# Performance work log

Hardware: AMD Instinct MI355X
Metric: run time of the kernel (lower is better)

The kernel has to match this reference:

```python
import jax, jax.numpy as jnp
import numpy as np

N_EMBD = 1024
N_EXPERTS = 8
TOP_K = 2
D_FF = 4 * N_EMBD


def setup_inputs() -> dict:
    key = jax.random.key(0)
    ks = jax.random.split(key, 6)
    B, S = 4, 2048
    s = 1.0 / np.sqrt(N_EMBD)
    sf = 1.0 / np.sqrt(D_FF)
    x = jax.random.normal(ks[0], (B, S, N_EMBD), dtype=jnp.float32)
    router_w = jax.random.uniform(ks[1], (N_EMBD, N_EXPERTS), minval=-s, maxval=s, dtype=jnp.float32)
    wfc = jax.random.uniform(ks[2], (N_EXPERTS, N_EMBD, D_FF), minval=-s, maxval=s, dtype=jnp.float32)
    bfc = jax.random.uniform(ks[3], (N_EXPERTS, D_FF), minval=-s, maxval=s, dtype=jnp.float32)
    wproj = jax.random.uniform(ks[4], (N_EXPERTS, D_FF, N_EMBD), minval=-sf, maxval=sf, dtype=jnp.float32)
    bproj = jax.random.uniform(ks[5], (N_EXPERTS, N_EMBD), minval=-sf, maxval=sf, dtype=jnp.float32)
    return {"x": x, "router_w": router_w, "wfc": wfc, "bfc": bfc, "wproj": wproj, "bproj": bproj}


def reference(x, router_w, wfc, bfc, wproj, bproj):
    B, S, D = x.shape
    E = wfc.shape[0]
    xf = x.reshape(-1, D)  # [N, D] tokens
    logits = xf @ router_w  # [N, E]
    probs = jax.nn.softmax(logits.astype(jnp.float32), axis=-1)
    w, sel = jax.lax.top_k(probs, TOP_K)  # [N, K]
    w = w / jnp.sum(w, axis=-1, keepdims=True)  # norm_topk_prob
    w = w.astype(x.dtype)
    out = jnp.zeros_like(xf)
    for e in range(E):
        # per-token gate for expert e (0 if not routed here) -- same math as
        # gather -> MLP -> weighted scatter-add in the original
        gate = jnp.sum(jnp.where(sel == e, w, jnp.zeros_like(w)), axis=-1)  # [N]
        h = jax.nn.gelu(xf @ wfc[e] + bfc[e], approximate=False)  # [N, 4D]
        y = h @ wproj[e] + bproj[e]  # [N, D]
        out = out + gate[:, None] * y
    return out.reshape(B, S, D)
```

## Files before the change

### kernel.cpp

```cpp
#include <hip/hip_runtime.h>
#include <hip/hip_bf16.h>


#define N_TOK 8192
#define DMODEL 1024
#define NEXP 8
#define DFF 4096
#define CAP 8192
#define MAXW 136

typedef __attribute__((ext_vector_type(8))) short short8;
typedef __attribute__((ext_vector_type(4))) float f32x4;

#define GLOAD_LDS16(g, l)                                              \
  __builtin_amdgcn_global_load_lds(                                    \
      (const __attribute__((address_space(1))) unsigned int*)(g),      \
      (__attribute__((address_space(3))) unsigned int*)(l), 16, 0, 0)

__device__ __forceinline__ unsigned short f2bf(float f) {
  unsigned u = __float_as_uint(f);
  return (unsigned short)((u + 0x7FFFu + ((u >> 16) & 1u)) >> 16);
}

__device__ __forceinline__ float gelu_f(float v) {
  return 0.5f * v * (1.0f + erff(v * 0.70710678118654752f));
}

__global__ void router_k(const float* __restrict__ x, const float* __restrict__ rw,
                         int* __restrict__ cnt, int* __restrict__ tok,
                         float* __restrict__ gate, unsigned short* __restrict__ xb) {
  int lane = threadIdx.x & 63;
  int t = blockIdx.x * 4 + (threadIdx.x >> 6);
  const float* xr = x + (size_t)t * DMODEL;
  unsigned short* xbr = xb + (size_t)t * DMODEL;
  float p[8];
#pragma unroll
  for (int e = 0; e < 8; ++e) p[e] = 0.0f;
#pragma unroll
  for (int j = 0; j < DMODEL / 64; ++j) {
    int i = lane + j * 64;
    float xv = xr[i];
    xbr[i] = f2bf(xv);
    const float4* r = (const float4*)(rw + (size_t)i * 8);
    float4 a = r[0], b = r[1];
    p[0] += xv * a.x; p[1] += xv * a.y; p[2] += xv * a.z; p[3] += xv * a.w;
    p[4] += xv * b.x; p[5] += xv * b.y; p[6] += xv * b.z; p[7] += xv * b.w;
  }
#pragma unroll
  for (int e = 0; e < 8; ++e) {
#pragma unroll
    for (int off = 32; off; off >>= 1) p[e] += __shfl_xor(p[e], off, 64);
  }
  if (lane == 0) {
    int e1 = 0;
#pragma unroll
    for (int e = 1; e < 8; ++e) if (p[e] > p[e1]) e1 = e;
    int e2 = (e1 == 0) ? 1 : 0;
#pragma unroll
    for (int e = 0; e < 8; ++e) if (e != e1 && p[e] > p[e2]) e2 = e;
    float w1 = 1.0f / (1.0f + expf(p[e2] - p[e1]));
    float w2 = 1.0f - w1;
    int s1 = atomicAdd(&cnt[e1], 1);
    tok[e1 * CAP + s1] = t; gate[e1 * CAP + s1] = w1;
    int s2 = atomicAdd(&cnt[e2], 1);
    tok[e2 * CAP + s2] = t; gate[e2 * CAP + s2] = w2;
  }
}

__global__ void prefix_k(const int* __restrict__ cnt, int* __restrict__ off,
                         int* __restrict__ nwork, int* __restrict__ wl) {
  if (threadIdx.x == 0 && blockIdx.x == 0) {
    int s = 0, n = 0;
    for (int e = 0; e < NEXP; ++e) {
      off[e] = s;
      int ntile = (cnt[e] + 127) >> 7;
      for (int mt = 0; mt < ntile; ++mt) wl[n++] = (e << 16) | mt;
      s += cnt[e];
    }
    nwork[0] = n;
  }
}

__global__ __launch_bounds__(256) void cvt_wt_k(const float* __restrict__ W,
                                                unsigned short* __restrict__ WT,
                                                int K, int N) {
  __shared__ float ls[64][68];
  int b = blockIdx.x;
  int nkt = K >> 6, nnt = N >> 6;
  int kt = b % nkt;
  int nt = (b / nkt) % nnt;
  int e = b / (nkt * nnt);
  const float* Wb = W + (size_t)e * K * N + (size_t)(kt * 64) * N + nt * 64;
  int t = threadIdx.x;
  int nn = (t & 15) * 4, kr = t >> 4;
#pragma unroll
  for (int i = 0; i < 4; ++i) {
    float4 v = *(const float4*)(Wb + (size_t)(kr + 16 * i) * N + nn);
    *(float4*)&ls[kr + 16 * i][nn] = v;
  }
  __syncthreads();
  int on = t >> 2, kc = (t & 3) * 16;
  unsigned short* dst = WT + (size_t)e * N * K + (size_t)(nt * 64 + on) * K + kt * 64 + kc;
  short8 r0, r1;
#pragma unroll
  for (int j = 0; j < 8; ++j) r0[j] = (short)f2bf(ls[kc + j][on]);
#pragma unroll
  for (int j = 0; j < 8; ++j) r1[j] = (short)f2bf(ls[kc + 8 + j][on]);
  *(short8*)dst = r0;
  *(short8*)(dst + 8) = r1;
}

#define STAGE(buf, kk)                                              \
  do {                                                              \
    GLOAD_LDS16(gA0 + (kk), &As[buf][(w * 32 + lr) * 32 + lc]);     \
    GLOAD_LDS16(gA1 + (kk), &As[buf][(w * 32 + 16 + lr) * 32 + lc]);\
    GLOAD_LDS16(gB0 + (kk), &Bs[buf][(w * 32 + lr) * 32 + lc]);     \
    GLOAD_LDS16(gB1 + (kk), &Bs[buf][(w * 32 + 16 + lr) * 32 + lc]);\
  } while (0)

#define COMPUTE(buf)                                                            \
  do {                                                                          \
    short8 af[4], bfv[4];                                                       \
    _Pragma("unroll") for (int i = 0; i < 4; ++i)                               \
        af[i] = *(const short8*)&As[buf][(wr * 64 + i * 16 + fr) * 32 + g * 8]; \
    _Pragma("unroll") for (int i = 0; i < 4; ++i)                               \
        bfv[i] = *(const short8*)&Bs[buf][(wc * 64 + i * 16 + fr) * 32 + g * 8];\
    _Pragma("unroll") for (int mi = 0; mi < 4; ++mi)                            \
        _Pragma("unroll") for (int ni = 0; ni < 4; ++ni)                        \
            acc[mi][ni] = __builtin_amdgcn_mfma_f32_16x16x32_bf16(              \
                af[mi], bfv[ni], acc[mi][ni], 0, 0, 0);                         \
  } while (0)

#define WAITV(n) asm volatile("s_waitcnt vmcnt(" #n ")" ::: "memory")
#define BAR() __builtin_amdgcn_s_barrier()

#define KLOOP(KTOT)                                                 \
  STAGE(0, 0);                                                      \
  STAGE(1, 32);                                                     \
  STAGE(2, 64);                                                     \
  {                                                                 \
    int cur = 0;                                                    \
    _Pragma("unroll 1") for (int k0 = 0; k0 + 96 < (KTOT); k0 += 32) {\
      WAITV(8);                                                     \
      BAR();                                                        \
      COMPUTE(cur);                                                 \
      BAR();                                                        \
      STAGE(cur, k0 + 96);                                          \
      cur = (cur == 2) ? 0 : cur + 1;                               \
    }                                                               \
    WAITV(8);                                                       \
    BAR();                                                          \
    COMPUTE(cur);                                                   \
    cur = (cur == 2) ? 0 : cur + 1;                                 \
    WAITV(4);                                                       \
    BAR();                                                          \
    COMPUTE(cur);                                                   \
    cur = (cur == 2) ? 0 : cur + 1;                                 \
    WAITV(0);                                                       \
    BAR();                                                          \
    COMPUTE(cur);                                                   \
  }

__global__ __launch_bounds__(256, 3) void gemm1a_k(
    const unsigned short* __restrict__ xb, const unsigned short* __restrict__ wT,
    const float* __restrict__ bfc, const int* __restrict__ cnt,
    const int* __restrict__ off, const int* __restrict__ tok,
    const int* __restrict__ nwork, const int* __restrict__ wl,
    unsigned short* __restrict__ h) {
  int bid = (int)(blockIdx.x & 7) * ((int)gridDim.x >> 3) + (int)(blockIdx.x >> 3);
  int widx = bid % MAXW;
  int nt = bid / MAXW;
  if (widx >= nwork[0]) return;
  int wle = wl[widx];
  int e = wle >> 16;
  int mt = wle & 0xffff;
  int Me = cnt[e];
  int base = off[e];
  int n0 = nt * 128;

  __shared__ __align__(16) unsigned short As[3][128 * 32];
  __shared__ __align__(16) unsigned short Bs[3][128 * 32];

  int tid = threadIdx.x;
  int lane = tid & 63, w = tid >> 6;
  int lr = lane >> 2;
  int lc = (lane & 3) * 8;

  int ar0i = mt * 128 + w * 32 + lr;
  int ar1i = ar0i + 16;
  int t0 = tok[e * CAP + ((ar0i < Me) ? ar0i : (Me - 1))];
  int t1 = tok[e * CAP + ((ar1i < Me) ? ar1i : (Me - 1))];
  const unsigned short* gA0 = xb + (size_t)t0 * DMODEL + lc;
  const unsigned short* gA1 = xb + (size_t)t1 * DMODEL + lc;
  const unsigned short* gB0 = wT + ((size_t)e * DFF + n0 + w * 32 + lr) * DMODEL + lc;
  const unsigned short* gB1 = gB0 + (size_t)16 * DMODEL;

  int wr = w >> 1, wc = w & 1;
  int g = lane >> 4, fr = lane & 15;

  f32x4 acc[4][4];
#pragma unroll
  for (int i = 0; i < 4; ++i)
#pragma unroll
    for (int j = 0; j < 4; ++j) acc[i][j] = (f32x4)0.0f;

  KLOOP(DMODEL);

#pragma unroll
  for (int mi = 0; mi < 4; ++mi) {
    int rl = wr * 64 + mi * 16 + g * 4;
#pragma unroll
    for (int i = 0; i < 4; ++i) {
      int r = mt * 128 + rl + i;
      if (r < Me) {
        unsigned short* hrow = h + (size_t)(base + r) * DFF;
#pragma unroll
        for (int ni = 0; ni < 4; ++ni) {
          int col = n0 + wc * 64 + ni * 16 + fr;
          float v = acc[mi][ni][i] + bfc[e * DFF + col];
          hrow[col] = f2bf(gelu_f(v));
        }
      }
    }
  }
}

__global__ __launch_bounds__(256, 3) void gemm2a_k(
    const unsigned short* __restrict__ h, const unsigned short* __restrict__ wT,
    const float* __restrict__ bproj, const int* __restrict__ cnt,
    const int* __restrict__ off, const int* __restrict__ tok,
    const int* __restrict__ nwork, const int* __restrict__ wl,
    const float* __restrict__ gate, float* __restrict__ out) {
  int bid = (int)(blockIdx.x & 7) * ((int)gridDim.x >> 3) + (int)(blockIdx.x >> 3);
  int widx = bid % MAXW;
  int nt = bid / MAXW;
  if (widx >= nwork[0]) return;
  int wle = wl[widx];
  int e = wle >> 16;
  int mt = wle & 0xffff;
  int Me = cnt[e];
  int base = off[e];
  int n0 = nt * 128;

  __shared__ __align__(16) unsigned short As[3][128 * 32];
  __shared__ __align__(16) unsigned short Bs[3][128 * 32];

  int tid = threadIdx.x;
  int lane = tid & 63, w = tid >> 6;
  int lr = lane >> 2;
  int lc = (lane & 3) * 8;

  const unsigned short* gA0 = h + (size_t)(base + mt * 128 + w * 32 + lr) * DFF + lc;
  const unsigned short* gA1 = gA0 + (size_t)16 * DFF;
  const unsigned short* gB0 = wT + ((size_t)e * DMODEL + n0 + w * 32 + lr) * DFF + lc;
  const unsigned short* gB1 = gB0 + (size_t)16 * DFF;

  int wr = w >> 1, wc = w & 1;
  int g = lane >> 4, fr = lane & 15;

  f32x4 acc[4][4];
#pragma unroll
  for (int i = 0; i < 4; ++i)
#pragma unroll
    for (int j = 0; j < 4; ++j) acc[i][j] = (f32x4)0.0f;

  KLOOP(DFF);

#pragma unroll
  for (int mi = 0; mi < 4; ++mi) {
    int rl = wr * 64 + mi * 16 + g * 4;
#pragma unroll
    for (int i = 0; i < 4; ++i) {
      int r = mt * 128 + rl + i;
      if (r < Me) {
        int tkn = tok[e * CAP + r];
        float gv = gate[e * CAP + r];
        float* orow = out + (size_t)tkn * DMODEL;
#pragma unroll
        for (int ni = 0; ni < 4; ++ni) {
          int col = n0 + wc * 64 + ni * 16 + fr;
          float v = acc[mi][ni][i] + bproj[e * DMODEL + col];
          atomicAdd(orow + col, gv * v);
        }
      }
    }
  }
}

extern "C" void kernel_launch(void* const* d_in, const int* in_sizes, int n_in,
                              void* d_out, int out_size, void* d_ws, size_t ws_size,
                              hipStream_t stream) {
  const float* x = (const float*)d_in[0];
  const float* rw = (const float*)d_in[1];
  const float* wfc = (const float*)d_in[2];
  const float* bfc = (const float*)d_in[3];
  const float* wproj = (const float*)d_in[4];
  const float* bproj = (const float*)d_in[5];
  float* out = (float*)d_out;

  char* ws = (char*)d_ws;
  int* cnt = (int*)ws;
  int* off_ = (int*)(ws + 64);
  int* nwork = (int*)(ws + 128);
  int* wl = (int*)(ws + 256);
  int* tok = (int*)(ws + 4096);
  float* gate = (float*)(ws + 4096 + (size_t)NEXP * CAP * 4);
  size_t HOFF = 4096 + 2 * (size_t)NEXP * CAP * 4;
  unsigned short* h = (unsigned short*)(ws + HOFF);
  size_t HSZ = (size_t)(16384 + 128) * DFF * 2;
  size_t XOFF = HOFF + HSZ;
  size_t WOFF = XOFF + (size_t)N_TOK * DMODEL * 2;
  unsigned short* xb = (unsigned short*)(ws + XOFF);
  unsigned short* wT = (unsigned short*)(ws + WOFF);

  hipMemsetAsync(cnt, 0, 128, stream);
  hipMemsetAsync(out, 0, (size_t)out_size * 4, stream);
  router_k<<<N_TOK / 4, 256, 0, stream>>>(x, rw, cnt, tok, gate, xb);
  prefix_k<<<1, 64, 0, stream>>>(cnt, off_, nwork, wl);
  cvt_wt_k<<<NEXP * (DMODEL / 64) * (DFF / 64), 256, 0, stream>>>(wfc, wT, DMODEL, DFF);
  gemm1a_k<<<MAXW * 32, 256, 0, stream>>>(xb, wT, bfc, cnt, off_, tok, nwork, wl, h);
  cvt_wt_k<<<NEXP * (DFF / 64) * (DMODEL / 64), 256, 0, stream>>>(wproj, wT, DFF, DMODEL);
  gemm2a_k<<<MAXW * 8, 256, 0, stream>>>(h, wT, bproj, cnt, off_, tok, nwork, wl, gate, out);
}
```

Before: 827.0 us.

## Use 512-thread GEMM blocks with 8 waves and reorder tile indexing

Both expert GEMM kernels now run 512 threads (8 waves in a 2x4 grid) per 128x128 tile. Each wave computes a 64x32 sub-tile, which halves accumulator registers per wave and lets each thread issue one A and one B async load per stage, with the vmcnt waits adjusted to match. Block indexing now walks N-tiles fastest within a work item, so blocks sharing the same A rows run close together. When the workspace is large enough, both weight conversions go to separate buffers and run before the GEMMs. The cost is more LDS fragment reads per MFMA and heavier barrier synchronisation across 8 waves.

```diff
diff --git a/kernel.cpp b/kernel.cpp
--- a/kernel.cpp
+++ b/kernel.cpp
@@ -110,23 +110,21 @@
   *(short8*)(dst + 8) = r1;
 }
 
-#define STAGE(buf, kk)                                              \
-  do {                                                              \
-    GLOAD_LDS16(gA0 + (kk), &As[buf][(w * 32 + lr) * 32 + lc]);     \
-    GLOAD_LDS16(gA1 + (kk), &As[buf][(w * 32 + 16 + lr) * 32 + lc]);\
-    GLOAD_LDS16(gB0 + (kk), &Bs[buf][(w * 32 + lr) * 32 + lc]);     \
-    GLOAD_LDS16(gB1 + (kk), &Bs[buf][(w * 32 + 16 + lr) * 32 + lc]);\
+#define STAGE(buf, kk)                                          \
+  do {                                                          \
+    GLOAD_LDS16(gA + (kk), &As[buf][(tid >> 2) * 32 + lc]);     \
+    GLOAD_LDS16(gB + (kk), &Bs[buf][(tid >> 2) * 32 + lc]);     \
   } while (0)
 
 #define COMPUTE(buf)                                                            \
   do {                                                                          \
-    short8 af[4], bfv[4];                                                       \
+    short8 af[4], bfv[2];                                                       \
     _Pragma("unroll") for (int i = 0; i < 4; ++i)                               \
         af[i] = *(const short8*)&As[buf][(wr * 64 + i * 16 + fr) * 32 + g * 8]; \
-    _Pragma("unroll") for (int i = 0; i < 4; ++i)                               \
-        bfv[i] = *(const short8*)&Bs[buf][(wc * 64 + i * 16 + fr) * 32 + g * 8];\
+    _Pragma("unroll") for (int i = 0; i < 2; ++i)                               \
+        bfv[i] = *(const short8*)&Bs[buf][(wc * 32 + i * 16 + fr) * 32 + g * 8];\
     _Pragma("unroll") for (int mi = 0; mi < 4; ++mi)                            \
-        _Pragma("unroll") for (int ni = 0; ni < 4; ++ni)                        \
+        _Pragma("unroll") for (int ni = 0; ni < 2; ++ni)                        \
             acc[mi][ni] = __builtin_amdgcn_mfma_f32_16x16x32_bf16(              \
                 af[mi], bfv[ni], acc[mi][ni], 0, 0, 0);                         \
   } while (0)
@@ -141,18 +139,18 @@
   {                                                                 \
     int cur = 0;                                                    \
     _Pragma("unroll 1") for (int k0 = 0; k0 + 96 < (KTOT); k0 += 32) {\
-      WAITV(8);                                                     \
+      WAITV(4);                                                     \
       BAR();                                                        \
       COMPUTE(cur);                                                 \
       BAR();                                                        \
       STAGE(cur, k0 + 96);                                          \
       cur = (cur == 2) ? 0 : cur + 1;                               \
     }                                                               \
-    WAITV(8);                                                       \
+    WAITV(4);                                                       \
     BAR();                                                          \
     COMPUTE(cur);                                                   \
     cur = (cur == 2) ? 0 : cur + 1;                                 \
-    WAITV(4);                                                       \
+    WAITV(2);                                                       \
     BAR();                                                          \
     COMPUTE(cur);                                                   \
     cur = (cur == 2) ? 0 : cur + 1;                                 \
@@ -161,15 +159,16 @@
     COMPUTE(cur);                                                   \
   }
 
-__global__ __launch_bounds__(256, 3) void gemm1a_k(
+#define NT1 32
+__global__ __launch_bounds__(512, 4) void gemm1a_k(
     const unsigned short* __restrict__ xb, const unsigned short* __restrict__ wT,
     const float* __restrict__ bfc, const int* __restrict__ cnt,
     const int* __restrict__ off, const int* __restrict__ tok,
     const int* __restrict__ nwork, const int* __restrict__ wl,
     unsigned short* __restrict__ h) {
   int bid = (int)(blockIdx.x & 7) * ((int)gridDim.x >> 3) + (int)(blockIdx.x >> 3);
-  int widx = bid % MAXW;
-  int nt = bid / MAXW;
+  int widx = bid / NT1;
+  int nt = bid % NT1;
   if (widx >= nwork[0]) return;
   int wle = wl[widx];
   int e = wle >> 16;
@@ -183,26 +182,21 @@
 
   int tid = threadIdx.x;
   int lane = tid & 63, w = tid >> 6;
-  int lr = lane >> 2;
-  int lc = (lane & 3) * 8;
-
-  int ar0i = mt * 128 + w * 32 + lr;
-  int ar1i = ar0i + 16;
-  int t0 = tok[e * CAP + ((ar0i < Me) ? ar0i : (Me - 1))];
-  int t1 = tok[e * CAP + ((ar1i < Me) ? ar1i : (Me - 1))];
-  const unsigned short* gA0 = xb + (size_t)t0 * DMODEL + lc;
-  const unsigned short* gA1 = xb + (size_t)t1 * DMODEL + lc;
-  const unsigned short* gB0 = wT + ((size_t)e * DFF + n0 + w * 32 + lr) * DMODEL + lc;
-  const unsigned short* gB1 = gB0 + (size_t)16 * DMODEL;
-
-  int wr = w >> 1, wc = w & 1;
+  int lc = (tid & 3) * 8;
+
+  int ari = mt * 128 + (tid >> 2);
+  int t0 = tok[e * CAP + ((ari < Me) ? ari : (Me - 1))];
+  const unsigned short* gA = xb + (size_t)t0 * DMODEL + lc;
+  const unsigned short* gB = wT + ((size_t)e * DFF + n0 + (tid >> 2)) * DMODEL + lc;
+
+  int wr = w >> 2, wc = w & 3;
   int g = lane >> 4, fr = lane & 15;
 
-  f32x4 acc[4][4];
+  f32x4 acc[4][2];
 #pragma unroll
   for (int i = 0; i < 4; ++i)
 #pragma unroll
-    for (int j = 0; j < 4; ++j) acc[i][j] = (f32x4)0.0f;
+    for (int j = 0; j < 2; ++j) acc[i][j] = (f32x4)0.0f;
 
   KLOOP(DMODEL);
 
@@ -215,8 +209,8 @@
       if (r < Me) {
         unsigned short* hrow = h + (size_t)(base + r) * DFF;
 #pragma unroll
-        for (int ni = 0; ni < 4; ++ni) {
-          int col = n0 + wc * 64 + ni * 16 + fr;
+        for (int ni = 0; ni < 2; ++ni) {
+          int col = n0 + wc * 32 + ni * 16 + fr;
           float v = acc[mi][ni][i] + bfc[e * DFF + col];
           hrow[col] = f2bf(gelu_f(v));
         }
@@ -225,15 +219,16 @@
   }
 }
 
-__global__ __launch_bounds__(256, 3) void gemm2a_k(
+#define NT2 8
+__global__ __launch_bounds__(512, 4) void gemm2a_k(
     const unsigned short* __restrict__ h, const unsigned short* __restrict__ wT,
     const float* __restrict__ bproj, const int* __restrict__ cnt,
     const int* __restrict__ off, const int* __restrict__ tok,
     const int* __restrict__ nwork, const int* __restrict__ wl,
     const float* __restrict__ gate, float* __restrict__ out) {
   int bid = (int)(blockIdx.x & 7) * ((int)gridDim.x >> 3) + (int)(blockIdx.x >> 3);
-  int widx = bid % MAXW;
-  int nt = bid / MAXW;
+  int widx = bid / NT2;
+  int nt = bid % NT2;
   if (widx >= nwork[0]) return;
   int wle = wl[widx];
   int e = wle >> 16;
@@ -247,22 +242,19 @@
 
   int tid = threadIdx.x;
   int lane = tid & 63, w = tid >> 6;
-  int lr = lane >> 2;
-  int lc = (lane & 3) * 8;
-
-  const unsigned short* gA0 = h + (size_t)(base + mt * 128 + w * 32 + lr) * DFF + lc;
-  const unsigned short* gA1 = gA0 + (size_t)16 * DFF;
-  const unsigned short* gB0 = wT + ((size_t)e * DMODEL + n0 + w * 32 + lr) * DFF + lc;
-  const unsigned short* gB1 = gB0 + (size_t)16 * DFF;
-
-  int wr = w >> 1, wc = w & 1;
+  int lc = (tid & 3) * 8;
+
+  const unsigned short* gA = h + (size_t)(base + mt * 128 + (tid >> 2)) * DFF + lc;
+  const unsigned short* gB = wT + ((size_t)e * DMODEL + n0 + (tid >> 2)) * DFF + lc;
+
+  int wr = w >> 2, wc = w & 3;
   int g = lane >> 4, fr = lane & 15;
 
-  f32x4 acc[4][4];
+  f32x4 acc[4][2];
 #pragma unroll
   for (int i = 0; i < 4; ++i)
 #pragma unroll
-    for (int j = 0; j < 4; ++j) acc[i][j] = (f32x4)0.0f;
+    for (int j = 0; j < 2; ++j) acc[i][j] = (f32x4)0.0f;
 
   KLOOP(DFF);
 
@@ -277,8 +269,8 @@
         float gv = gate[e * CAP + r];
         float* orow = out + (size_t)tkn * DMODEL;
 #pragma unroll
-        for (int ni = 0; ni < 4; ++ni) {
-          int col = n0 + wc * 64 + ni * 16 + fr;
+        for (int ni = 0; ni < 2; ++ni) {
+          int col = n0 + wc * 32 + ni * 16 + fr;
           float v = acc[mi][ni][i] + bproj[e * DMODEL + col];
           atomicAdd(orow + col, gv * v);
         }
@@ -310,15 +302,25 @@
   size_t HSZ = (size_t)(16384 + 128) * DFF * 2;
   size_t XOFF = HOFF + HSZ;
   size_t WOFF = XOFF + (size_t)N_TOK * DMODEL * 2;
+  size_t WSZ = (size_t)NEXP * DFF * DMODEL * 2;
   unsigned short* xb = (unsigned short*)(ws + XOFF);
-  unsigned short* wT = (unsigned short*)(ws + WOFF);
+  unsigned short* wT1 = (unsigned short*)(ws + WOFF);
 
   hipMemsetAsync(cnt, 0, 128, stream);
   hipMemsetAsync(out, 0, (size_t)out_size * 4, stream);
   router_k<<<N_TOK / 4, 256, 0, stream>>>(x, rw, cnt, tok, gate, xb);
   prefix_k<<<1, 64, 0, stream>>>(cnt, off_, nwork, wl);
-  cvt_wt_k<<<NEXP * (DMODEL / 64) * (DFF / 64), 256, 0, stream>>>(wfc, wT, DMODEL, DFF);
-  gemm1a_k<<<MAXW * 32, 256, 0, stream>>>(xb, wT, bfc, cnt, off_, tok, nwork, wl, h);
-  cvt_wt_k<<<NEXP * (DFF / 64) * (DMODEL / 64), 256, 0, stream>>>(wproj, wT, DFF, DMODEL);
-  gemm2a_k<<<MAXW * 8, 256, 0, stream>>>(h, wT, bproj, cnt, off_, tok, nwork, wl, gate, out);
-}
+
+  if (ws_size >= WOFF + 2 * WSZ) {
+    unsigned short* wT2 = (unsigned short*)(ws + WOFF + WSZ);
+    cvt_wt_k<<<NEXP * (DMODEL / 64) * (DFF / 64), 256, 0, stream>>>(wfc, wT1, DMODEL, DFF);
+    cvt_wt_k<<<NEXP * (DFF / 64) * (DMODEL / 64), 256, 0, stream>>>(wproj, wT2, DFF, DMODEL);
+    gemm1a_k<<<MAXW * NT1, 512, 0, stream>>>(xb, wT1, bfc, cnt, off_, tok, nwork, wl, h);
+    gemm2a_k<<<MAXW * NT2, 512, 0, stream>>>(h, wT2, bproj, cnt, off_, tok, nwork, wl, gate, out);
+  } else {
+    cvt_wt_k<<<NEXP * (DMODEL / 64) * (DFF / 64), 256, 0, stream>>>(wfc, wT1, DMODEL, DFF);
+    gemm1a_k<<<MAXW * NT1, 512, 0, stream>>>(xb, wT1, bfc, cnt, off_, tok, nwork, wl, h);
+    cvt_wt_k<<<NEXP * (DFF / 64) * (DMODEL / 64), 256, 0, stream>>>(wproj, wT1, DFF, DMODEL);
+    gemm2a_k<<<MAXW * NT2, 512, 0, stream>>>(h, wT1, bproj, cnt, off_, tok, nwork, wl, gate, out);
+  }
+}
```

After: 768.9 us. -7.0%, faster.
